# Performance work log

Hardware: AMD Instinct MI355X
Metric: run time of the kernel (lower is better)

The kernel has to match this reference:

```python
import jax, jax.numpy as jnp
import numpy as np

N, E, D, H, L, FF = 50000, 500000, 128, 8, 2, 512
HD = D // H  # head dim = 16


def setup_inputs() -> dict:
    key = jax.random.key(0)
    ks = jax.random.split(key, 16)
    inp = {
        "x": jax.random.normal(ks[0], (N, D), jnp.float32),
        "edge_index": jax.random.randint(ks[1], (2, E), 0, N, jnp.int32),
    }
    def w(k, shape, fan_in):
        return jax.random.normal(k, shape, jnp.float32) / np.float32(np.sqrt(fan_in))
    inp["Wq"] = w(ks[2], (L, D, D), D)
    inp["Wk"] = w(ks[3], (L, D, D), D)
    inp["Wv"] = w(ks[4], (L, D, D), D)
    inp["Wo"] = w(ks[5], (L, D, D), D)
    inp["Wpos"] = w(ks[6], (L, D, D), D)
    inp["Wdeg"] = w(ks[7], (L, 1, D), 1)
    inp["W1"] = w(ks[8], (L, D, FF), D)
    inp["W2"] = w(ks[9], (L, FF, D), FF)
    for name, shape in [("bq", (L, D)), ("bk", (L, D)), ("bv", (L, D)),
                        ("bo", (L, D)), ("bpos", (L, D)), ("bdeg", (L, D)),
                        ("ln1_b", (L, D)), ("ln2_b", (L, D)),
                        ("b1", (L, FF)), ("b2", (L, D))]:
        inp[name] = jnp.zeros(shape, jnp.float32)
    inp["ln1_g"] = jnp.ones((L, D), jnp.float32)
    inp["ln2_g"] = jnp.ones((L, D), jnp.float32)
    return inp


def _layernorm(x, g, b):
    mu = jnp.mean(x, axis=-1, keepdims=True)
    var = jnp.mean(jnp.square(x - mu), axis=-1, keepdims=True)
    return (x - mu) * jax.lax.rsqrt(var + 1e-5) * g + b


def _forward(edge_index, x, Wq, bq, Wk, bk, Wv, bv, Wo, bo, Wpos, bpos,
             Wdeg, bdeg, ln1_g, ln1_b, ln2_g, ln2_b, W1, b1, W2, b2):
    n = x.shape[0]
    loops = jnp.arange(n, dtype=edge_index.dtype)
    src = jnp.concatenate([edge_index[0], loops])  # [E+N]
    dst = jnp.concatenate([edge_index[1], loops])  # [E+N]
    scale = np.float32(np.sqrt(HD))
    for l in range(L):
        # pre-attention LayerNorm
        xn = _layernorm(x, ln1_g[l], ln1_b[l])
        # positional encoding: x + proj(x) + deg_proj(standardized degree)
        deg = jax.ops.segment_sum(jnp.ones_like(src, dtype=x.dtype), src, num_segments=n)
        deg = (deg - deg.mean()) / (jnp.std(deg, ddof=1) + 1e-6)
        pos = xn @ Wpos[l] + bpos[l] + deg[:, None] * Wdeg[l][0] + bdeg[l]
        xp = xn + pos
        # per-node QKV projections (linear => identical to per-edge projection)
        q = (xp @ Wq[l] + bq[l]).reshape(n, H, HD)
        k = (xp @ Wk[l] + bk[l]).reshape(n, H, HD)
        v = (xp @ Wv[l] + bv[l]).reshape(n, H, HD)
        # per-edge attention logits  [E+N, H]
        att = jnp.einsum('ehd,ehd->eh', q[dst], k[src]) / scale
        att = jnp.nan_to_num(jnp.clip(att, -50.0, 50.0), nan=0.0, posinf=50.0, neginf=-50.0)
        # segment softmax over destination nodes (every node has a self loop)
        m = jax.ops.segment_max(att, dst, num_segments=n)        # [N, H]
        ex = jnp.exp(att - m[dst])
        s = jax.ops.segment_sum(ex, dst, num_segments=n)
        alpha = ex / (s[dst] + 1e-16)                             # [E+N, H]
        # weighted aggregation + output projection
        msg = (v[src] * alpha[:, :, None]).reshape(-1, D)         # [E+N, D]
        aggr = jax.ops.segment_sum(msg, dst, num_segments=n)      # [N, D]
        x = x + (aggr @ Wo[l] + bo[l])
        # FFN sublayer
        h = jax.nn.gelu(_layernorm(x, ln2_g[l], ln2_b[l]) @ W1[l] + b1[l], approximate=False)
        x = x + (h @ W2[l] + b2[l])
    return x


def reference(x, edge_index, Wq, bq, Wk, bk, Wv, bv, Wo, bo, Wpos, bpos,
              Wdeg, bdeg, ln1_g, ln1_b, ln2_g, ln2_b, W1, b1, W2, b2):
    return _forward(edge_index, x, Wq, bq, Wk, bk, Wv, bv, Wo, bo, Wpos, bpos,
                    Wdeg, bdeg, ln1_g, ln1_b, ln2_g, ln2_b, W1, b1, W2, b2)
```

## Files before the change

### kernel.cpp

```cpp
#include <hip/hip_runtime.h>
#include <hip/hip_bf16.h>
#include <hip/hip_fp16.h>
#include <math.h>

#define DMODEL 128
#define NHEAD 8
#define HEADD 16
#define NLAYER 2
#define FFDIM 512
#define MPAD 50048
#define QKVW 384

using short8 = __attribute__((ext_vector_type(8))) short;
using half8  = __attribute__((ext_vector_type(8))) _Float16;
using f32x4  = __attribute__((ext_vector_type(4))) float;

static __device__ __forceinline__ unsigned short f2h(float f) {
    __half h = __float2half(f);
    unsigned short u; __builtin_memcpy(&u, &h, 2); return u;
}
static __device__ __forceinline__ float h2f(unsigned short u) {
    __half h; __builtin_memcpy(&h, &u, 2); return __half2float(h);
}
static __device__ __forceinline__ half8 s2h8(short8 s) {
    half8 h; __builtin_memcpy(&h, &s, 16); return h;
}
static __device__ __forceinline__ f32x4 MFMAH(short8 a, short8 b, f32x4 c) {
    return __builtin_amdgcn_mfma_f32_16x16x32_f16(s2h8(a), s2h8(b), c, 0, 0, 0);
}
static __device__ __forceinline__ float gelu_fast(float v) {
    float u = v * (0.7978845608f + 0.0356774081f * v * v);
    float t = 1.0f - 2.0f / (1.0f + __expf(2.0f * u));
    return 0.5f * v * (1.0f + t);
}

__global__ __launch_bounds__(256)
void ln_kernel(const float* __restrict__ x, const float* __restrict__ g,
               const float* __restrict__ b, unsigned short* __restrict__ out, int n)
{
    int wave = threadIdx.x >> 6;
    int lane = threadIdx.x & 63;
    int row  = blockIdx.x * 4 + wave;
    if (row >= n) return;
    float2 xv = *(const float2*)(x + (size_t)row * DMODEL + lane * 2);
    float s  = xv.x + xv.y;
    float ss = xv.x * xv.x + xv.y * xv.y;
    #pragma unroll
    for (int d = 1; d < 64; d <<= 1) {
        s  += __shfl_xor(s, d);
        ss += __shfl_xor(ss, d);
    }
    float mu   = s * (1.0f / 128.0f);
    float var  = ss * (1.0f / 128.0f) - mu * mu;
    float rstd = rsqrtf(var + 1e-5f);
    float2 gv = *(const float2*)(g + lane * 2);
    float2 bv = *(const float2*)(b + lane * 2);
    ushort2 o;
    o.x = f2h((xv.x - mu) * rstd * gv.x + bv.x);
    o.y = f2h((xv.y - mu) * rstd * gv.y + bv.y);
    *(ushort2*)(out + (size_t)row * DMODEL + lane * 2) = o;
}

__global__ void wconv(const float* __restrict__ W, unsigned short* __restrict__ Wt,
                      int K, int N, int total, int NR, int rowOff)
{
    int i = blockIdx.x * 256 + threadIdx.x;
    if (i >= total) return;
    int kn = K * N;
    int l = i / kn;
    int r = i - l * kn;
    int k = r / N;
    int nn = r - k * N;
    Wt[(size_t)l * NR * K + (size_t)(rowOff + nn) * K + k] = f2h(W[i]);
}

template<int MODE, int KCH, int TPB>
__global__ __launch_bounds__(256)
void gemm_bres(const unsigned short* __restrict__ A, int strideA,
               const unsigned short* __restrict__ Bt, int strideB,
               const float* __restrict__ bias, const float* __restrict__ bias2,
               const float* __restrict__ bias3,
               const unsigned short* __restrict__ Rb,
               const float* __restrict__ degs, const float* __restrict__ wdeg,
               const float* __restrict__ bdeg,
               float* __restrict__ outf, unsigned short* __restrict__ outb,
               int outStride, int n)
{
    __shared__ __align__(16) unsigned short As[64 * 130];
    __shared__ __align__(16) unsigned short Bs[128 * 130];

    const int tid  = threadIdx.x;
    const int wave = tid >> 6, lane = tid & 63;
    const int wr = wave >> 1, wc = wave & 1;
    const int quad = lane >> 4, l15 = lane & 15;
    const int bc = blockIdx.y * 128;

    f32x4 acc[2][4] = {};
    short8 bfr[4][4];
    short8 pr[4];

    {
        const int row0 = blockIdx.x * TPB * 64;
        #pragma unroll
        for (int c = 0; c < 4; ++c) {
            int g = tid + c * 256;
            int r = g >> 4, col8 = g & 15;
            pr[c] = *(const short8*)(A + (size_t)(row0 + r) * strideA + col8 * 8);
        }
    }

    for (int ky = 0; ky < KCH; ++ky) {
        const int kOff = ky * 128;
        #pragma unroll
        for (int c = 0; c < 8; ++c) {
            int g = tid + c * 256;
            int r = g >> 4, col8 = g & 15;
            *(short8*)&Bs[r * 130 + col8 * 8] =
                *(const short8*)(Bt + (size_t)(bc + r) * strideB + kOff + col8 * 8);
        }
        for (int t = 0; t < TPB; ++t) {
            #pragma unroll
            for (int c = 0; c < 4; ++c) {
                int g = tid + c * 256;
                int r = g >> 4, col8 = g & 15;
                *(short8*)&As[r * 130 + col8 * 8] = pr[c];
            }
            {
                int nt = t + 1, nky = ky;
                if (nt == TPB) { nt = 0; nky = ky + 1; }
                if (nky < KCH) {
                    const int nrow0 = (blockIdx.x * TPB + nt) * 64;
                    const int nkOff = nky * 128;
                    #pragma unroll
                    for (int c = 0; c < 4; ++c) {
                        int g = tid + c * 256;
                        int r = g >> 4, col8 = g & 15;
                        pr[c] = *(const short8*)(A + (size_t)(nrow0 + r) * strideA + nkOff + col8 * 8);
                    }
                }
            }
            __syncthreads();
            if (t == 0) {
                #pragma unroll
                for (int j = 0; j < 4; ++j)
                    #pragma unroll
                    for (int ks = 0; ks < 4; ++ks)
                        bfr[j][ks] = *(const short8*)&Bs[(wc * 64 + j * 16 + l15) * 130 + (ks * 4 + quad) * 8];
            }
            if (KCH == 1) {
                #pragma unroll
                for (int i = 0; i < 2; ++i)
                    #pragma unroll
                    for (int j = 0; j < 4; ++j)
                        acc[i][j] = f32x4{0.f, 0.f, 0.f, 0.f};
            }
            short8 af[2][4];
            #pragma unroll
            for (int i = 0; i < 2; ++i)
                #pragma unroll
                for (int ks = 0; ks < 4; ++ks)
                    af[i][ks] = *(const short8*)&As[(wr * 32 + i * 16 + l15) * 130 + (ks * 4 + quad) * 8];
            #pragma unroll
            for (int ks = 0; ks < 4; ++ks)
                #pragma unroll
                for (int i = 0; i < 2; ++i)
                    #pragma unroll
                    for (int j = 0; j < 4; ++j)
                        acc[i][j] = MFMAH(af[i][ks], bfr[j][ks], acc[i][j]);

            if (KCH == 1) {
                const int row0 = (blockIdx.x * TPB + t) * 64;
                #pragma unroll
                for (int i = 0; i < 2; ++i) {
                    #pragma unroll
                    for (int rr = 0; rr < 4; ++rr) {
                        size_t gr = (size_t)row0 + wr * 32 + i * 16 + quad * 4 + rr;
                        if (gr >= (size_t)n) continue;
                        #pragma unroll
                        for (int j = 0; j < 4; ++j) {
                            int col = wc * 64 + j * 16 + l15;
                            int gc  = bc + col;
                            float val = acc[i][j][rr];
                            if (MODE == 0) {
                                int sec = blockIdx.y;
                                const float* bp = (sec == 0) ? bias : (sec == 1 ? bias2 : bias3);
                                val += bp[col];
                                int idx = (sec == 0) ? col
                                        : (128 + ((col >> 1) << 2) + ((sec - 1) << 1) + (col & 1));
                                outb[gr * (size_t)QKVW + idx] = f2h(val);
                            } else if (MODE == 1) {
                                float* px = outf + gr * (size_t)outStride + gc;
                                *px = *px + val + bias[gc];
                            } else if (MODE == 2) {
                                val = gelu_fast(val + bias[gc]);
                                outb[gr * (size_t)outStride + gc] = f2h(val);
                            } else if (MODE == 3) {
                                val += bias[gc] + h2f(Rb[gr * (size_t)outStride + gc])
                                     + degs[gr] * wdeg[gc] + bdeg[gc];
                                outb[gr * (size_t)outStride + gc] = f2h(val);
                            }
                        }
                    }
                }
            }
            __syncthreads();
        }
    }

    if (KCH > 1) {
        const int row0 = blockIdx.x * TPB * 64;
        #pragma unroll
        for (int i = 0; i < 2; ++i) {
            #pragma unroll
            for (int rr = 0; rr < 4; ++rr) {
                size_t gr = (size_t)row0 + wr * 32 + i * 16 + quad * 4 + rr;
                if (gr >= (size_t)n) continue;
                #pragma unroll
                for (int j = 0; j < 4; ++j) {
                    int col = wc * 64 + j * 16 + l15;
                    int gc  = bc + col;
                    float val = acc[i][j][rr];
                    if (MODE == 1) {
                        float* px = outf + gr * (size_t)outStride + gc;
                        *px = *px + val + bias[gc];
                    }
                }
            }
        }
    }
}

__global__ void deg_init(float* __restrict__ deg, int n)
{
    int i = blockIdx.x * 256 + threadIdx.x;
    if (i < n) deg[i] = 1.0f;
}

__global__ void deg_count(const int* __restrict__ src, float* __restrict__ deg, int e)
{
    int i = blockIdx.x * 256 + threadIdx.x;
    if (i < e) atomicAdd(&deg[src[i]], 1.0f);
}

__global__ __launch_bounds__(256)
void deg_var(const float* __restrict__ deg, float* __restrict__ stats, float mean, int n)
{
    float acc = 0.f;
    for (int i = blockIdx.x * blockDim.x + threadIdx.x; i < n; i += gridDim.x * blockDim.x) {
        float d = deg[i] - mean;
        acc += d * d;
    }
    #pragma unroll
    for (int d = 1; d < 64; d <<= 1) acc += __shfl_xor(acc, d);
    __shared__ float wsum[4];
    int lane = threadIdx.x & 63, wv = threadIdx.x >> 6;
    if (lane == 0) wsum[wv] = acc;
    __syncthreads();
    if (threadIdx.x == 0) atomicAdd(stats, wsum[0] + wsum[1] + wsum[2] + wsum[3]);
}

__global__ void deg_norm(const float* __restrict__ deg, const float* __restrict__ stats,
                         float* __restrict__ degs, float mean, int n)
{
    int i = blockIdx.x * 256 + threadIdx.x;
    if (i >= n) return;
    float sd = sqrtf(stats[0] / (float)(n - 1));
    degs[i] = (deg[i] - mean) / (sd + 1e-6f);
}

__global__ void csr_count(const int* __restrict__ ei, int* __restrict__ counts, int e, int n)
{
    int i = blockIdx.x * 256 + threadIdx.x;
    if (i >= e + n) return;
    int d = (i < e) ? ei[e + i] : (i - e);
    atomicAdd(&counts[d], 1);
}

__global__ __launch_bounds__(256)
void scan_block(const int* __restrict__ in, int* __restrict__ out,
                int* __restrict__ sums, int n)
{
    __shared__ int buf[2][256];
    int t = threadIdx.x;
    int i = blockIdx.x * 256 + t;
    int v = (i < n) ? in[i] : 0;
    buf[0][t] = v;
    __syncthreads();
    int cur = 0;
    #pragma unroll
    for (int d = 1; d < 256; d <<= 1) {
        int val = buf[cur][t] + ((t >= d) ? buf[cur][t - d] : 0);
        buf[cur ^ 1][t] = val;
        cur ^= 1;
        __syncthreads();
    }
    if (i < n) out[i] = buf[cur][t] - v;
    if (t == 255 && sums) sums[blockIdx.x] = buf[cur][255];
}

__global__ void scan_add(int* __restrict__ offs, const int* __restrict__ carry, int n)
{
    int i = blockIdx.x * 256 + threadIdx.x;
    if (i < n) offs[i] += carry[blockIdx.x];
}

__global__ void csr_fill(const int* __restrict__ ei, const int* __restrict__ offs,
                         int* __restrict__ cursor, int* __restrict__ csr_src, int e, int n)
{
    int i = blockIdx.x * 256 + threadIdx.x;
    if (i >= e + n) return;
    int d, s;
    if (i < e) { s = ei[i]; d = ei[e + i]; }
    else       { s = d = i - e; }
    int pos = offs[d] + atomicAdd(&cursor[d], 1);
    csr_src[pos] = s;
}

__global__ __launch_bounds__(256)
void attn_kernel(const unsigned short* __restrict__ qkv,
                 const int* __restrict__ csr_src, const int* __restrict__ offs,
                 const int* __restrict__ counts,
                 unsigned short* __restrict__ aggr, int n)
{
    int wave = threadIdx.x >> 6;
    int lane = threadIdx.x & 63;
    int node = blockIdx.x * 4 + wave;
    if (node >= n) return;

    ushort2 qu = *(const ushort2*)(qkv + (size_t)node * QKVW + lane * 2);
    float qx = h2f(qu.x), qy = h2f(qu.y);
    int beg = offs[node], cnt = counts[node];

    float m = -1e30f, s = 0.f, ax = 0.f, ay = 0.f;
    ushort4 kvA = {0,0,0,0}, kvB = {0,0,0,0};
    if (cnt > 1) {
        int j0 = csr_src[beg], j1 = csr_src[beg + 1];
        kvA = *(const ushort4*)(qkv + (size_t)j0 * QKVW + DMODEL + lane * 4);
        kvB = *(const ushort4*)(qkv + (size_t)j1 * QKVW + DMODEL + lane * 4);
    } else {
        int j0 = csr_src[beg];
        kvA = *(const ushort4*)(qkv + (size_t)j0 * QKVW + DMODEL + lane * 4);
    }
    int t = 0;
    for (; t + 1 < cnt; t += 2) {
        ushort4 k0 = kvA, k1 = kvB;
        int rem = cnt - t - 2;
        if (rem >= 2) {
            int j0 = csr_src[beg + t + 2], j1 = csr_src[beg + t + 3];
            kvA = *(const ushort4*)(qkv + (size_t)j0 * QKVW + DMODEL + lane * 4);
            kvB = *(const ushort4*)(qkv + (size_t)j1 * QKVW + DMODEL + lane * 4);
        } else if (rem == 1) {
            int j0 = csr_src[beg + t + 2];
            kvA = *(const ushort4*)(qkv + (size_t)j0 * QKVW + DMODEL + lane * 4);
        }
        float p0 = qx * h2f(k0.x) + qy * h2f(k0.y);
        float p1 = qx * h2f(k1.x) + qy * h2f(k1.y);
        p0 += __shfl_xor(p0, 1); p1 += __shfl_xor(p1, 1);
        p0 += __shfl_xor(p0, 2); p1 += __shfl_xor(p1, 2);
        p0 += __shfl_xor(p0, 4); p1 += __shfl_xor(p1, 4);
        p0 *= 0.25f; p1 *= 0.25f;
        p0 = (p0 != p0) ? 0.f : fminf(fmaxf(p0, -50.f), 50.f);
        p1 = (p1 != p1) ? 0.f : fminf(fmaxf(p1, -50.f), 50.f);
        float nm = fmaxf(m, fmaxf(p0, p1));
        float sc = __expf(m - nm);
        float e0 = __expf(p0 - nm), e1 = __expf(p1 - nm);
        s  = s  * sc + e0 + e1;
        ax = ax * sc + e0 * h2f(k0.z) + e1 * h2f(k1.z);
        ay = ay * sc + e0 * h2f(k0.w) + e1 * h2f(k1.w);
        m = nm;
    }
    if (t < cnt) {
        float p0 = qx * h2f(kvA.x) + qy * h2f(kvA.y);
        p0 += __shfl_xor(p0, 1); p0 += __shfl_xor(p0, 2); p0 += __shfl_xor(p0, 4);
        p0 *= 0.25f;
        p0 = (p0 != p0) ? 0.f : fminf(fmaxf(p0, -50.f), 50.f);
        float nm = fmaxf(m, p0);
        float sc = __expf(m - nm), e0 = __expf(p0 - nm);
        s = s * sc + e0;
        ax = ax * sc + e0 * h2f(kvA.z);
        ay = ay * sc + e0 * h2f(kvA.w);
        m = nm;
    }
    float r = 1.0f / (s + 1e-16f);
    ushort2 o;
    o.x = f2h(ax * r);
    o.y = f2h(ay * r);
    *(ushort2*)(aggr + (size_t)node * DMODEL + lane * 2) = o;
}

extern "C" void kernel_launch(void* const* d_in, const int* in_sizes, int n_in,
                              void* d_out, int out_size, void* d_ws, size_t ws_size,
                              hipStream_t stream)
{
    const float* x_in  = (const float*)d_in[0];
    const int*   ei    = (const int*)d_in[1];
    const float* Wq    = (const float*)d_in[2];
    const float* Wk    = (const float*)d_in[3];
    const float* Wv    = (const float*)d_in[4];
    const float* Wo    = (const float*)d_in[5];
    const float* Wpos  = (const float*)d_in[6];
    const float* Wdeg  = (const float*)d_in[7];
    const float* W1    = (const float*)d_in[8];
    const float* W2    = (const float*)d_in[9];
    const float* bq    = (const float*)d_in[10];
    const float* bk    = (const float*)d_in[11];
    const float* bv    = (const float*)d_in[12];
    const float* bo    = (const float*)d_in[13];
    const float* bpos  = (const float*)d_in[14];
    const float* bdeg  = (const float*)d_in[15];
    const float* ln1_b = (const float*)d_in[16];
    const float* ln2_b = (const float*)d_in[17];
    const float* b1    = (const float*)d_in[18];
    const float* b2    = (const float*)d_in[19];
    const float* ln1_g = (const float*)d_in[20];
    const float* ln2_g = (const float*)d_in[21];

    const int n   = in_sizes[0] / DMODEL;
    const int e   = in_sizes[1] / 2;
    const int tot = e + n;

    float* x = (float*)d_out;

    char* p = (char*)d_ws;
    auto alloc = [&](size_t bytes) -> void* {
        void* r = (void*)p;
        p += (bytes + 255) & ~(size_t)255;
        return r;
    };
    float* deg     = (float*)alloc((size_t)n * 4);
    float* degs    = (float*)alloc((size_t)n * 4);
    float* stats   = (float*)alloc(256);
    int*   counts  = (int*)alloc((size_t)n * 4);
    int*   offs    = (int*)alloc((size_t)n * 4);
    int*   cursor  = (int*)alloc((size_t)n * 4);
    int*   bsums   = (int*)alloc(1024);
    int*   carry   = (int*)alloc(1024);
    int*   csr_src = (int*)alloc((size_t)tot * 4);
    unsigned short* xnb  = (unsigned short*)alloc((size_t)MPAD * DMODEL * 2);
    unsigned short* xp   = (unsigned short*)alloc((size_t)MPAD * DMODEL * 2);
    unsigned short* aggr = (unsigned short*)alloc((size_t)MPAD * DMODEL * 2);
    unsigned short* qkv  = (unsigned short*)alloc((size_t)MPAD * QKVW * 2);
    unsigned short* hb   = (unsigned short*)alloc((size_t)MPAD * FFDIM * 2);
    unsigned short* wqkvt = (unsigned short*)alloc((size_t)NLAYER * QKVW * DMODEL * 2);
    unsigned short* wot  = (unsigned short*)alloc((size_t)NLAYER * DMODEL * DMODEL * 2);
    unsigned short* wpt  = (unsigned short*)alloc((size_t)NLAYER * DMODEL * DMODEL * 2);
    unsigned short* w1t  = (unsigned short*)alloc((size_t)NLAYER * DMODEL * FFDIM * 2);
    unsigned short* w2t  = (unsigned short*)alloc((size_t)NLAYER * FFDIM * DMODEL * 2);

    const int nb_n = (n + 255) / 256;
    const int nb_e = (e + 255) / 256;
    const int nb_t = (tot + 255) / 256;
    const int nscan = nb_n;

    hipMemcpyAsync(x, x_in, (size_t)n * DMODEL * 4, hipMemcpyDeviceToDevice, stream);
    hipMemsetAsync(stats, 0, 256, stream);
    hipMemsetAsync(counts, 0, (size_t)n * 4, stream);
    hipMemsetAsync(cursor, 0, (size_t)n * 4, stream);

    {
        int tDD = NLAYER * DMODEL * DMODEL;
        int tW1 = NLAYER * DMODEL * FFDIM;
        wconv<<<(tDD + 255) / 256, 256, 0, stream>>>(Wq,   wqkvt, DMODEL, DMODEL, tDD, QKVW, 0);
        wconv<<<(tDD + 255) / 256, 256, 0, stream>>>(Wk,   wqkvt, DMODEL, DMODEL, tDD, QKVW, 128);
        wconv<<<(tDD + 255) / 256, 256, 0, stream>>>(Wv,   wqkvt, DMODEL, DMODEL, tDD, QKVW, 256);
        wconv<<<(tDD + 255) / 256, 256, 0, stream>>>(Wo,   wot, DMODEL, DMODEL, tDD, DMODEL, 0);
        wconv<<<(tDD + 255) / 256, 256, 0, stream>>>(Wpos, wpt, DMODEL, DMODEL, tDD, DMODEL, 0);
        wconv<<<(tW1 + 255) / 256, 256, 0, stream>>>(W1,   w1t, DMODEL, FFDIM,  tW1, FFDIM, 0);
        wconv<<<(tW1 + 255) / 256, 256, 0, stream>>>(W2,   w2t, FFDIM,  DMODEL, tW1, DMODEL, 0);
    }

    const float mean = (float)((double)tot / (double)n);
    deg_init<<<nb_n, 256, 0, stream>>>(deg, n);
    deg_count<<<nb_e, 256, 0, stream>>>(ei, deg, e);
    deg_var<<<196, 256, 0, stream>>>(deg, stats, mean, n);
    deg_norm<<<nb_n, 256, 0, stream>>>(deg, stats, degs, mean, n);

    csr_count<<<nb_t, 256, 0, stream>>>(ei, counts, e, n);
    scan_block<<<nscan, 256, 0, stream>>>(counts, offs, bsums, n);
    scan_block<<<1, 256, 0, stream>>>(bsums, carry, nullptr, nscan);
    scan_add<<<nscan, 256, 0, stream>>>(offs, carry, n);
    csr_fill<<<nb_t, 256, 0, stream>>>(ei, offs, cursor, csr_src, e, n);

    const int nTiles  = MPAD / 64;
    const int gx2     = nTiles / 2;
    const int ln_grid = (n + 3) / 4;

    for (int l = 0; l < NLAYER; ++l) {
        const size_t DD = (size_t)DMODEL * DMODEL;
        const float* wdeg = Wdeg + (size_t)l * DMODEL;
        const unsigned short* wqkv = wqkvt + (size_t)l * QKVW * DMODEL;
        const unsigned short* wo   = wot + l * DD;
        const unsigned short* wpos = wpt + l * DD;
        const unsigned short* w1   = w1t + (size_t)l * DMODEL * FFDIM;
        const unsigned short* w2   = w2t + (size_t)l * FFDIM * DMODEL;

        ln_kernel<<<ln_grid, 256, 0, stream>>>(x, ln1_g + l * DMODEL, ln1_b + l * DMODEL, xnb, n);
        gemm_bres<3, 1, 2><<<dim3(gx2, 1), 256, 0, stream>>>(
            xnb, DMODEL, wpos, DMODEL,
            bpos + l * DMODEL, nullptr, nullptr,
            xnb, degs, wdeg, bdeg + l * DMODEL,
            nullptr, xp, DMODEL, n);
        gemm_bres<0, 1, 2><<<dim3(gx2, 3), 256, 0, stream>>>(
            xp, DMODEL, wqkv, DMODEL,
            bq + l * DMODEL, bk + l * DMODEL, bv + l * DMODEL,
            nullptr, nullptr, nullptr, nullptr,
            nullptr, qkv, QKVW, n);
        attn_kernel<<<ln_grid, 256, 0, stream>>>(qkv, csr_src, offs, counts, aggr, n);
        gemm_bres<1, 1, 2><<<dim3(gx2, 1), 256, 0, stream>>>(
            aggr, DMODEL, wo, DMODEL,
            bo + l * DMODEL, nullptr, nullptr,
            nullptr, nullptr, nullptr, nullptr,
            x, nullptr, DMODEL, n);
        ln_kernel<<<ln_grid, 256, 0, stream>>>(x, ln2_g + l * DMODEL, ln2_b + l * DMODEL, xnb, n);
        gemm_bres<2, 1, 2><<<dim3(gx2, 4), 256, 0, stream>>>(
            xnb, DMODEL, w1, DMODEL,
            b1 + l * FFDIM, nullptr, nullptr,
            nullptr, nullptr, nullptr, nullptr,
            nullptr, hb, FFDIM, n);
        gemm_bres<1, 4, 1><<<dim3(nTiles, 1), 256, 0, stream>>>(
            hb, FFDIM, w2, FFDIM,
            b2 + l * DMODEL, nullptr, nullptr,
            nullptr, nullptr, nullptr, nullptr,
            x, nullptr, DMODEL, n);
    }
}
```

Baseline: 619.2 us.

## Fuse LayerNorm into residual GEMM epilogues and merge setup kernels

Adds a GEMM epilogue mode that applies the residual add and then LayerNorm over the full 128-wide row, using a shared-memory reduction across waves. The separate LayerNorm kernels after the Wo and W2 GEMMs go away, which removes an extra full read of x per LayerNorm. The setup work is also consolidated: the weight conversions become one kernel, the memsets and degree init become one kernel, and degree normalization moves into the positional GEMM epilogue. The attention loop is rewritten to process four edges per iteration with prefetching of the next group and no NaN check. The cost is an extra block sync and more register pressure in the GEMM epilogue.

```diff
diff --git a/kernel.cpp b/kernel.cpp
--- a/kernel.cpp
+++ b/kernel.cpp
@@ -61,17 +61,173 @@
     *(ushort2*)(out + (size_t)row * DMODEL + lane * 2) = o;
 }
 
-__global__ void wconv(const float* __restrict__ W, unsigned short* __restrict__ Wt,
-                      int K, int N, int total, int NR, int rowOff)
-{
+__global__ void wconv_all(const float* __restrict__ Wq, const float* __restrict__ Wk,
+                          const float* __restrict__ Wv, const float* __restrict__ Wo,
+                          const float* __restrict__ Wpos, const float* __restrict__ W1,
+                          const float* __restrict__ W2,
+                          unsigned short* __restrict__ wqkvt, unsigned short* __restrict__ wot,
+                          unsigned short* __restrict__ wpt, unsigned short* __restrict__ w1t,
+                          unsigned short* __restrict__ w2t)
+{
+    const int DD = NLAYER * DMODEL * DMODEL;
+    const int DF = NLAYER * DMODEL * FFDIM;
     int i = blockIdx.x * 256 + threadIdx.x;
-    if (i >= total) return;
-    int kn = K * N;
-    int l = i / kn;
-    int r = i - l * kn;
-    int k = r / N;
-    int nn = r - k * N;
-    Wt[(size_t)l * NR * K + (size_t)(rowOff + nn) * K + k] = f2h(W[i]);
+    if (i < 3 * DD) {
+        int w = i / DD, r = i - w * DD;
+        const float* src = (w == 0) ? Wq : (w == 1 ? Wk : Wv);
+        int l = r >> 14, rr = r & 16383;
+        int k = rr >> 7, nn = rr & 127;
+        wqkvt[(size_t)l * QKVW * DMODEL + (size_t)(w * 128 + nn) * DMODEL + k] = f2h(src[r]);
+    } else if (i < 5 * DD) {
+        int w = (i - 3 * DD) / DD, r = (i - 3 * DD) - w * DD;
+        const float* src = (w == 0) ? Wo : Wpos;
+        unsigned short* dst = (w == 0) ? wot : wpt;
+        int l = r >> 14, rr = r & 16383;
+        int k = rr >> 7, nn = rr & 127;
+        dst[(size_t)l * DMODEL * DMODEL + (size_t)nn * DMODEL + k] = f2h(src[r]);
+    } else if (i < 5 * DD + DF) {
+        int r = i - 5 * DD;
+        int l = r >> 16, rr = r & 65535;
+        int k = rr >> 9, nn = rr & 511;
+        w1t[(size_t)l * FFDIM * DMODEL + (size_t)nn * DMODEL + k] = f2h(W1[r]);
+    } else if (i < 5 * DD + 2 * DF) {
+        int r = i - 5 * DD - DF;
+        int l = r >> 16, rr = r & 65535;
+        int k = rr >> 7, nn = rr & 127;
+        w2t[(size_t)l * DMODEL * FFDIM + (size_t)nn * FFDIM + k] = f2h(W2[r]);
+    }
+}
+
+__global__ void init_all(float* __restrict__ deg, int* __restrict__ counts,
+                         int* __restrict__ cursor, float* __restrict__ stats, int n)
+{
+    int i = blockIdx.x * 256 + threadIdx.x;
+    if (i < n) { deg[i] = 1.0f; counts[i] = 0; cursor[i] = 0; }
+    if (i == 0) stats[0] = 0.f;
+}
+
+__global__ void deg_count(const int* __restrict__ src, float* __restrict__ deg, int e)
+{
+    int i = blockIdx.x * 256 + threadIdx.x;
+    if (i < e) atomicAdd(&deg[src[i]], 1.0f);
+}
+
+__global__ __launch_bounds__(256)
+void deg_var(const float* __restrict__ deg, float* __restrict__ stats, float mean, int n)
+{
+    float acc = 0.f;
+    for (int i = blockIdx.x * blockDim.x + threadIdx.x; i < n; i += gridDim.x * blockDim.x) {
+        float d = deg[i] - mean;
+        acc += d * d;
+    }
+    #pragma unroll
+    for (int d = 1; d < 64; d <<= 1) acc += __shfl_xor(acc, d);
+    __shared__ float wsum[4];
+    int lane = threadIdx.x & 63, wv = threadIdx.x >> 6;
+    if (lane == 0) wsum[wv] = acc;
+    __syncthreads();
+    if (threadIdx.x == 0) atomicAdd(stats, wsum[0] + wsum[1] + wsum[2] + wsum[3]);
+}
+
+__global__ void csr_count(const int* __restrict__ ei, int* __restrict__ counts, int e, int n)
+{
+    int i = blockIdx.x * 256 + threadIdx.x;
+    if (i >= e + n) return;
+    int d = (i < e) ? ei[e + i] : (i - e);
+    atomicAdd(&counts[d], 1);
+}
+
+__global__ __launch_bounds__(256)
+void scan_block(const int* __restrict__ in, int* __restrict__ out,
+                int* __restrict__ sums, int n)
+{
+    __shared__ int buf[2][256];
+    int t = threadIdx.x;
+    int i = blockIdx.x * 256 + t;
+    int v = (i < n) ? in[i] : 0;
+    buf[0][t] = v;
+    __syncthreads();
+    int cur = 0;
+    #pragma unroll
+    for (int d = 1; d < 256; d <<= 1) {
+        int val = buf[cur][t] + ((t >= d) ? buf[cur][t - d] : 0);
+        buf[cur ^ 1][t] = val;
+        cur ^= 1;
+        __syncthreads();
+    }
+    if (i < n) out[i] = buf[cur][t] - v;
+    if (t == 255 && sums) sums[blockIdx.x] = buf[cur][255];
+}
+
+__global__ void scan_add(int* __restrict__ offs, const int* __restrict__ carry, int n)
+{
+    int i = blockIdx.x * 256 + threadIdx.x;
+    if (i < n) offs[i] += carry[blockIdx.x];
+}
+
+__global__ void csr_fill(const int* __restrict__ ei, const int* __restrict__ offs,
+                         int* __restrict__ cursor, int* __restrict__ csr_src, int e, int n)
+{
+    int i = blockIdx.x * 256 + threadIdx.x;
+    if (i >= e + n) return;
+    int d, s;
+    if (i < e) { s = ei[i]; d = ei[e + i]; }
+    else       { s = d = i - e; }
+    int pos = offs[d] + atomicAdd(&cursor[d], 1);
+    csr_src[pos] = s;
+}
+
+static __device__ __forceinline__ void ep_resln(
+    f32x4 (&acc)[2][4], float* sm, int row0,
+    int wr, int wc, int quad, int l15,
+    const float* __restrict__ bias, const float* __restrict__ g,
+    const float* __restrict__ bb,
+    float* __restrict__ x, unsigned short* __restrict__ lnout, int n)
+{
+    #pragma unroll
+    for (int i = 0; i < 2; ++i) {
+        #pragma unroll
+        for (int rr = 0; rr < 4; ++rr) {
+            int rl = wr * 32 + i * 16 + quad * 4 + rr;
+            size_t gr = (size_t)row0 + rl;
+            float ps = 0.f, pq = 0.f;
+            #pragma unroll
+            for (int j = 0; j < 4; ++j) {
+                int gc = wc * 64 + j * 16 + l15;
+                float xv = (gr < (size_t)n) ? x[gr * DMODEL + gc] : 0.f;
+                float v = acc[i][j][rr] + bias[gc] + xv;
+                acc[i][j][rr] = v;
+                ps += v; pq += v * v;
+            }
+            ps += __shfl_xor(ps, 1); pq += __shfl_xor(pq, 1);
+            ps += __shfl_xor(ps, 2); pq += __shfl_xor(pq, 2);
+            ps += __shfl_xor(ps, 4); pq += __shfl_xor(pq, 4);
+            ps += __shfl_xor(ps, 8); pq += __shfl_xor(pq, 8);
+            if (l15 == 0) { sm[(rl * 2 + wc) * 2 + 0] = ps; sm[(rl * 2 + wc) * 2 + 1] = pq; }
+        }
+    }
+    __syncthreads();
+    #pragma unroll
+    for (int i = 0; i < 2; ++i) {
+        #pragma unroll
+        for (int rr = 0; rr < 4; ++rr) {
+            int rl = wr * 32 + i * 16 + quad * 4 + rr;
+            size_t gr = (size_t)row0 + rl;
+            if (gr >= (size_t)n) continue;
+            float su = sm[(rl * 2 + 0) * 2 + 0] + sm[(rl * 2 + 1) * 2 + 0];
+            float sq = sm[(rl * 2 + 0) * 2 + 1] + sm[(rl * 2 + 1) * 2 + 1];
+            float mu   = su * (1.f / 128.f);
+            float var  = sq * (1.f / 128.f) - mu * mu;
+            float rstd = rsqrtf(var + 1e-5f);
+            #pragma unroll
+            for (int j = 0; j < 4; ++j) {
+                int gc = wc * 64 + j * 16 + l15;
+                float v = acc[i][j][rr];
+                x[gr * DMODEL + gc] = v;
+                lnout[gr * DMODEL + gc] = f2h((v - mu) * rstd * g[gc] + bb[gc]);
+            }
+        }
+    }
 }
 
 template<int MODE, int KCH, int TPB>
@@ -81,13 +237,15 @@
                const float* __restrict__ bias, const float* __restrict__ bias2,
                const float* __restrict__ bias3,
                const unsigned short* __restrict__ Rb,
-               const float* __restrict__ degs, const float* __restrict__ wdeg,
-               const float* __restrict__ bdeg,
+               const float* __restrict__ deg, const float* __restrict__ stats, float mean,
+               const float* __restrict__ wdeg, const float* __restrict__ bdeg,
+               const float* __restrict__ lng, const float* __restrict__ lnb,
                float* __restrict__ outf, unsigned short* __restrict__ outb,
                int outStride, int n)
 {
     __shared__ __align__(16) unsigned short As[64 * 130];
     __shared__ __align__(16) unsigned short Bs[128 * 130];
+    __shared__ float sm[64 * 2 * 2];
 
     const int tid  = threadIdx.x;
     const int wave = tid >> 6, lane = tid & 63;
@@ -170,34 +328,41 @@
 
             if (KCH == 1) {
                 const int row0 = (blockIdx.x * TPB + t) * 64;
-                #pragma unroll
-                for (int i = 0; i < 2; ++i) {
+                if (MODE == 5) {
+                    ep_resln(acc, sm, row0, wr, wc, quad, l15, bias, lng, lnb, outf, outb, n);
+                } else {
+                    float sdv = 0.f;
+                    if (MODE == 3) sdv = sqrtf(stats[0] / (float)(n - 1)) + 1e-6f;
                     #pragma unroll
-                    for (int rr = 0; rr < 4; ++rr) {
-                        size_t gr = (size_t)row0 + wr * 32 + i * 16 + quad * 4 + rr;
-                        if (gr >= (size_t)n) continue;
+                    for (int i = 0; i < 2; ++i) {
                         #pragma unroll
-                        for (int j = 0; j < 4; ++j) {
-                            int col = wc * 64 + j * 16 + l15;
-                            int gc  = bc + col;
-                            float val = acc[i][j][rr];
-                            if (MODE == 0) {
-                                int sec = blockIdx.y;
-                                const float* bp = (sec == 0) ? bias : (sec == 1 ? bias2 : bias3);
-                                val += bp[col];
-                                int idx = (sec == 0) ? col
-                                        : (128 + ((col >> 1) << 2) + ((sec - 1) << 1) + (col & 1));
-                                outb[gr * (size_t)QKVW + idx] = f2h(val);
-                            } else if (MODE == 1) {
-                                float* px = outf + gr * (size_t)outStride + gc;
-                                *px = *px + val + bias[gc];
-                            } else if (MODE == 2) {
-                                val = gelu_fast(val + bias[gc]);
-                                outb[gr * (size_t)outStride + gc] = f2h(val);
-                            } else if (MODE == 3) {
-                                val += bias[gc] + h2f(Rb[gr * (size_t)outStride + gc])
-                                     + degs[gr] * wdeg[gc] + bdeg[gc];
-                                outb[gr * (size_t)outStride + gc] = f2h(val);
+                        for (int rr = 0; rr < 4; ++rr) {
+                            size_t gr = (size_t)row0 + wr * 32 + i * 16 + quad * 4 + rr;
+                            if (gr >= (size_t)n) continue;
+                            #pragma unroll
+                            for (int j = 0; j < 4; ++j) {
+                                int col = wc * 64 + j * 16 + l15;
+                                int gc  = bc + col;
+                                float val = acc[i][j][rr];
+                                if (MODE == 0) {
+                                    int sec = blockIdx.y;
+                                    const float* bp = (sec == 0) ? bias : (sec == 1 ? bias2 : bias3);
+                                    val += bp[col];
+                                    int idx = (sec == 0) ? col
+                                            : (128 + ((col >> 1) << 2) + ((sec - 1) << 1) + (col & 1));
+                                    outb[gr * (size_t)QKVW + idx] = f2h(val);
+                                } else if (MODE == 1) {
+                                    float* px = outf + gr * (size_t)outStride + gc;
+                                    *px = *px + val + bias[gc];
+                                } else if (MODE == 2) {
+                                    val = gelu_fast(val + bias[gc]);
+                                    outb[gr * (size_t)outStride + gc] = f2h(val);
+                                } else if (MODE == 3) {
+                                    float dg = (deg[gr] - mean) / sdv;
+                                    val += bias[gc] + h2f(Rb[gr * (size_t)outStride + gc])
+                                         + dg * wdeg[gc] + bdeg[gc];
+                                    outb[gr * (size_t)outStride + gc] = f2h(val);
+                                }
                             }
                         }
                     }
@@ -209,111 +374,28 @@
 
     if (KCH > 1) {
         const int row0 = blockIdx.x * TPB * 64;
-        #pragma unroll
-        for (int i = 0; i < 2; ++i) {
+        if (MODE == 5) {
+            ep_resln(acc, sm, row0, wr, wc, quad, l15, bias, lng, lnb, outf, outb, n);
+        } else {
             #pragma unroll
-            for (int rr = 0; rr < 4; ++rr) {
-                size_t gr = (size_t)row0 + wr * 32 + i * 16 + quad * 4 + rr;
-                if (gr >= (size_t)n) continue;
+            for (int i = 0; i < 2; ++i) {
                 #pragma unroll
-                for (int j = 0; j < 4; ++j) {
-                    int col = wc * 64 + j * 16 + l15;
-                    int gc  = bc + col;
-                    float val = acc[i][j][rr];
-                    if (MODE == 1) {
-                        float* px = outf + gr * (size_t)outStride + gc;
-                        *px = *px + val + bias[gc];
+                for (int rr = 0; rr < 4; ++rr) {
+                    size_t gr = (size_t)row0 + wr * 32 + i * 16 + quad * 4 + rr;
+                    if (gr >= (size_t)n) continue;
+                    #pragma unroll
+                    for (int j = 0; j < 4; ++j) {
+                        int col = wc * 64 + j * 16 + l15;
+                        int gc  = bc + col;
+                        if (MODE == 1) {
+                            float* px = outf + gr * (size_t)outStride + gc;
+                            *px = *px + acc[i][j][rr] + bias[gc];
+                        }
                     }
                 }
             }
         }
     }
-}
-
-__global__ void deg_init(float* __restrict__ deg, int n)
-{
-    int i = blockIdx.x * 256 + threadIdx.x;
-    if (i < n) deg[i] = 1.0f;
-}
-
-__global__ void deg_count(const int* __restrict__ src, float* __restrict__ deg, int e)
-{
-    int i = blockIdx.x * 256 + threadIdx.x;
-    if (i < e) atomicAdd(&deg[src[i]], 1.0f);
-}
-
-__global__ __launch_bounds__(256)
-void deg_var(const float* __restrict__ deg, float* __restrict__ stats, float mean, int n)
-{
-    float acc = 0.f;
-    for (int i = blockIdx.x * blockDim.x + threadIdx.x; i < n; i += gridDim.x * blockDim.x) {
-        float d = deg[i] - mean;
-        acc += d * d;
-    }
-    #pragma unroll
-    for (int d = 1; d < 64; d <<= 1) acc += __shfl_xor(acc, d);
-    __shared__ float wsum[4];
-    int lane = threadIdx.x & 63, wv = threadIdx.x >> 6;
-    if (lane == 0) wsum[wv] = acc;
-    __syncthreads();
-    if (threadIdx.x == 0) atomicAdd(stats, wsum[0] + wsum[1] + wsum[2] + wsum[3]);
-}
-
-__global__ void deg_norm(const float* __restrict__ deg, const float* __restrict__ stats,
-                         float* __restrict__ degs, float mean, int n)
-{
-    int i = blockIdx.x * 256 + threadIdx.x;
-    if (i >= n) return;
-    float sd = sqrtf(stats[0] / (float)(n - 1));
-    degs[i] = (deg[i] - mean) / (sd + 1e-6f);
-}
-
-__global__ void csr_count(const int* __restrict__ ei, int* __restrict__ counts, int e, int n)
-{
-    int i = blockIdx.x * 256 + threadIdx.x;
-    if (i >= e + n) return;
-    int d = (i < e) ? ei[e + i] : (i - e);
-    atomicAdd(&counts[d], 1);
-}
-
-__global__ __launch_bounds__(256)
-void scan_block(const int* __restrict__ in, int* __restrict__ out,
-                int* __restrict__ sums, int n)
-{
-    __shared__ int buf[2][256];
-    int t = threadIdx.x;
-    int i = blockIdx.x * 256 + t;
-    int v = (i < n) ? in[i] : 0;
-    buf[0][t] = v;
-    __syncthreads();
-    int cur = 0;
-    #pragma unroll
-    for (int d = 1; d < 256; d <<= 1) {
-        int val = buf[cur][t] + ((t >= d) ? buf[cur][t - d] : 0);
-        buf[cur ^ 1][t] = val;
-        cur ^= 1;
-        __syncthreads();
-    }
-    if (i < n) out[i] = buf[cur][t] - v;
-    if (t == 255 && sums) sums[blockIdx.x] = buf[cur][255];
-}
-
-__global__ void scan_add(int* __restrict__ offs, const int* __restrict__ carry, int n)
-{
-    int i = blockIdx.x * 256 + threadIdx.x;
-    if (i < n) offs[i] += carry[blockIdx.x];
-}
-
-__global__ void csr_fill(const int* __restrict__ ei, const int* __restrict__ offs,
-                         int* __restrict__ cursor, int* __restrict__ csr_src, int e, int n)
-{
-    int i = blockIdx.x * 256 + threadIdx.x;
-    if (i >= e + n) return;
-    int d, s;
-    if (i < e) { s = ei[i]; d = ei[e + i]; }
-    else       { s = d = i - e; }
-    int pos = offs[d] + atomicAdd(&cursor[d], 1);
-    csr_src[pos] = s;
 }
 
 __global__ __launch_bounds__(256)
@@ -331,60 +413,64 @@
     float qx = h2f(qu.x), qy = h2f(qu.y);
     int beg = offs[node], cnt = counts[node];
 
+    const unsigned short* base = qkv + DMODEL + lane * 4;
+    auto LKV = [&](int t) -> ushort4 {
+        return *(const ushort4*)(base + (size_t)csr_src[beg + t] * QKVW);
+    };
+
     float m = -1e30f, s = 0.f, ax = 0.f, ay = 0.f;
-    ushort4 kvA = {0,0,0,0}, kvB = {0,0,0,0};
-    if (cnt > 1) {
-        int j0 = csr_src[beg], j1 = csr_src[beg + 1];
-        kvA = *(const ushort4*)(qkv + (size_t)j0 * QKVW + DMODEL + lane * 4);
-        kvB = *(const ushort4*)(qkv + (size_t)j1 * QKVW + DMODEL + lane * 4);
-    } else {
-        int j0 = csr_src[beg];
-        kvA = *(const ushort4*)(qkv + (size_t)j0 * QKVW + DMODEL + lane * 4);
-    }
+    ushort4 k0 = {0,0,0,0}, k1 = {0,0,0,0}, k2 = {0,0,0,0}, k3 = {0,0,0,0};
+    k0 = LKV(0);
+    if (cnt > 1) k1 = LKV(1);
+    if (cnt > 2) k2 = LKV(2);
+    if (cnt > 3) k3 = LKV(3);
+
     int t = 0;
-    for (; t + 1 < cnt; t += 2) {
-        ushort4 k0 = kvA, k1 = kvB;
-        int rem = cnt - t - 2;
-        if (rem >= 2) {
-            int j0 = csr_src[beg + t + 2], j1 = csr_src[beg + t + 3];
-            kvA = *(const ushort4*)(qkv + (size_t)j0 * QKVW + DMODEL + lane * 4);
-            kvB = *(const ushort4*)(qkv + (size_t)j1 * QKVW + DMODEL + lane * 4);
-        } else if (rem == 1) {
-            int j0 = csr_src[beg + t + 2];
-            kvA = *(const ushort4*)(qkv + (size_t)j0 * QKVW + DMODEL + lane * 4);
-        }
-        float p0 = qx * h2f(k0.x) + qy * h2f(k0.y);
-        float p1 = qx * h2f(k1.x) + qy * h2f(k1.y);
-        p0 += __shfl_xor(p0, 1); p1 += __shfl_xor(p1, 1);
-        p0 += __shfl_xor(p0, 2); p1 += __shfl_xor(p1, 2);
-        p0 += __shfl_xor(p0, 4); p1 += __shfl_xor(p1, 4);
-        p0 *= 0.25f; p1 *= 0.25f;
-        p0 = (p0 != p0) ? 0.f : fminf(fmaxf(p0, -50.f), 50.f);
-        p1 = (p1 != p1) ? 0.f : fminf(fmaxf(p1, -50.f), 50.f);
-        float nm = fmaxf(m, fmaxf(p0, p1));
+    for (; t + 4 <= cnt; t += 4) {
+        ushort4 c0 = k0, c1 = k1, c2 = k2, c3 = k3;
+        int rem = cnt - t - 4;
+        if (rem > 0) k0 = LKV(t + 4);
+        if (rem > 1) k1 = LKV(t + 5);
+        if (rem > 2) k2 = LKV(t + 6);
+        if (rem > 3) k3 = LKV(t + 7);
+        float p0 = qx * h2f(c0.x) + qy * h2f(c0.y);
+        float p1 = qx * h2f(c1.x) + qy * h2f(c1.y);
+        float p2 = qx * h2f(c2.x) + qy * h2f(c2.y);
+        float p3 = qx * h2f(c3.x) + qy * h2f(c3.y);
+        p0 += __shfl_xor(p0, 1); p1 += __shfl_xor(p1, 1); p2 += __shfl_xor(p2, 1); p3 += __shfl_xor(p3, 1);
+        p0 += __shfl_xor(p0, 2); p1 += __shfl_xor(p1, 2); p2 += __shfl_xor(p2, 2); p3 += __shfl_xor(p3, 2);
+        p0 += __shfl_xor(p0, 4); p1 += __shfl_xor(p1, 4); p2 += __shfl_xor(p2, 4); p3 += __shfl_xor(p3, 4);
+        p0 = fminf(fmaxf(p0 * 0.25f, -50.f), 50.f);
+        p1 = fminf(fmaxf(p1 * 0.25f, -50.f), 50.f);
+        p2 = fminf(fmaxf(p2 * 0.25f, -50.f), 50.f);
+        p3 = fminf(fmaxf(p3 * 0.25f, -50.f), 50.f);
+        float nm = fmaxf(m, fmaxf(fmaxf(p0, p1), fmaxf(p2, p3)));
         float sc = __expf(m - nm);
         float e0 = __expf(p0 - nm), e1 = __expf(p1 - nm);
-        s  = s  * sc + e0 + e1;
-        ax = ax * sc + e0 * h2f(k0.z) + e1 * h2f(k1.z);
-        ay = ay * sc + e0 * h2f(k0.w) + e1 * h2f(k1.w);
+        float e2 = __expf(p2 - nm), e3 = __expf(p3 - nm);
+        s  = s  * sc + ((e0 + e1) + (e2 + e3));
+        ax = ax * sc + e0 * h2f(c0.z) + e1 * h2f(c1.z) + e2 * h2f(c2.z) + e3 * h2f(c3.z);
+        ay = ay * sc + e0 * h2f(c0.w) + e1 * h2f(c1.w) + e2 * h2f(c2.w) + e3 * h2f(c3.w);
         m = nm;
     }
-    if (t < cnt) {
-        float p0 = qx * h2f(kvA.x) + qy * h2f(kvA.y);
-        p0 += __shfl_xor(p0, 1); p0 += __shfl_xor(p0, 2); p0 += __shfl_xor(p0, 4);
-        p0 *= 0.25f;
-        p0 = (p0 != p0) ? 0.f : fminf(fmaxf(p0, -50.f), 50.f);
-        float nm = fmaxf(m, p0);
-        float sc = __expf(m - nm), e0 = __expf(p0 - nm);
-        s = s * sc + e0;
-        ax = ax * sc + e0 * h2f(kvA.z);
-        ay = ay * sc + e0 * h2f(kvA.w);
-        m = nm;
-    }
-    float r = 1.0f / (s + 1e-16f);
+    int r = cnt - t;
+    #define ONE_EDGE(kc) do { \
+        float p = qx * h2f(kc.x) + qy * h2f(kc.y); \
+        p += __shfl_xor(p, 1); p += __shfl_xor(p, 2); p += __shfl_xor(p, 4); \
+        p = fminf(fmaxf(p * 0.25f, -50.f), 50.f); \
+        float nm = fmaxf(m, p); \
+        float sc = __expf(m - nm), e = __expf(p - nm); \
+        s = s * sc + e; ax = ax * sc + e * h2f(kc.z); ay = ay * sc + e * h2f(kc.w); \
+        m = nm; } while (0)
+    if (r > 0) ONE_EDGE(k0);
+    if (r > 1) ONE_EDGE(k1);
+    if (r > 2) ONE_EDGE(k2);
+    #undef ONE_EDGE
+
+    float rcp = 1.0f / (s + 1e-16f);
     ushort2 o;
-    o.x = f2h(ax * r);
-    o.y = f2h(ay * r);
+    o.x = f2h(ax * rcp);
+    o.y = f2h(ay * rcp);
     *(ushort2*)(aggr + (size_t)node * DMODEL + lane * 2) = o;
 }
 
@@ -428,7 +514,6 @@
         return r;
     };
     float* deg     = (float*)alloc((size_t)n * 4);
-    float* degs    = (float*)alloc((size_t)n * 4);
     float* stats   = (float*)alloc(256);
     int*   counts  = (int*)alloc((size_t)n * 4);
     int*   offs    = (int*)alloc((size_t)n * 4);
@@ -453,27 +538,17 @@
     const int nscan = nb_n;
 
     hipMemcpyAsync(x, x_in, (size_t)n * DMODEL * 4, hipMemcpyDeviceToDevice, stream);
-    hipMemsetAsync(stats, 0, 256, stream);
-    hipMemsetAsync(counts, 0, (size_t)n * 4, stream);
-    hipMemsetAsync(cursor, 0, (size_t)n * 4, stream);
 
     {
-        int tDD = NLAYER * DMODEL * DMODEL;
-        int tW1 = NLAYER * DMODEL * FFDIM;
-        wconv<<<(tDD + 255) / 256, 256, 0, stream>>>(Wq,   wqkvt, DMODEL, DMODEL, tDD, QKVW, 0);
-        wconv<<<(tDD + 255) / 256, 256, 0, stream>>>(Wk,   wqkvt, DMODEL, DMODEL, tDD, QKVW, 128);
-        wconv<<<(tDD + 255) / 256, 256, 0, stream>>>(Wv,   wqkvt, DMODEL, DMODEL, tDD, QKVW, 256);
-        wconv<<<(tDD + 255) / 256, 256, 0, stream>>>(Wo,   wot, DMODEL, DMODEL, tDD, DMODEL, 0);
-        wconv<<<(tDD + 255) / 256, 256, 0, stream>>>(Wpos, wpt, DMODEL, DMODEL, tDD, DMODEL, 0);
-        wconv<<<(tW1 + 255) / 256, 256, 0, stream>>>(W1,   w1t, DMODEL, FFDIM,  tW1, FFDIM, 0);
-        wconv<<<(tW1 + 255) / 256, 256, 0, stream>>>(W2,   w2t, FFDIM,  DMODEL, tW1, DMODEL, 0);
-    }
+        const int totalW = 5 * NLAYER * DMODEL * DMODEL + 2 * NLAYER * DMODEL * FFDIM;
+        wconv_all<<<(totalW + 255) / 256, 256, 0, stream>>>(Wq, Wk, Wv, Wo, Wpos, W1, W2,
+                                                            wqkvt, wot, wpt, w1t, w2t);
+    }
+    init_all<<<nb_n, 256, 0, stream>>>(deg, counts, cursor, stats, n);
 
     const float mean = (float)((double)tot / (double)n);
-    deg_init<<<nb_n, 256, 0, stream>>>(deg, n);
     deg_count<<<nb_e, 256, 0, stream>>>(ei, deg, e);
     deg_var<<<196, 256, 0, stream>>>(deg, stats, mean, n);
-    deg_norm<<<nb_n, 256, 0, stream>>>(deg, stats, degs, mean, n);
 
     csr_count<<<nb_t, 256, 0, stream>>>(ei, counts, e, n);
     scan_block<<<nscan, 256, 0, stream>>>(counts, offs, bsums, n);
@@ -484,6 +559,8 @@
     const int nTiles  = MPAD / 64;
     const int gx2     = nTiles / 2;
     const int ln_grid = (n + 3) / 4;
+
+    ln_kernel<<<ln_grid, 256, 0, stream>>>(x, ln1_g, ln1_b, xnb, n);
 
     for (int l = 0; l < NLAYER; ++l) {
         const size_t DD = (size_t)DMODEL * DMODEL;
@@ -494,33 +571,45 @@
         const unsigned short* w1   = w1t + (size_t)l * DMODEL * FFDIM;
         const unsigned short* w2   = w2t + (size_t)l * FFDIM * DMODEL;
 
-        ln_kernel<<<ln_grid, 256, 0, stream>>>(x, ln1_g + l * DMODEL, ln1_b + l * DMODEL, xnb, n);
         gemm_bres<3, 1, 2><<<dim3(gx2, 1), 256, 0, stream>>>(
             xnb, DMODEL, wpos, DMODEL,
             bpos + l * DMODEL, nullptr, nullptr,
-            xnb, degs, wdeg, bdeg + l * DMODEL,
+            xnb, deg, stats, mean, wdeg, bdeg + l * DMODEL,
+            nullptr, nullptr,
             nullptr, xp, DMODEL, n);
         gemm_bres<0, 1, 2><<<dim3(gx2, 3), 256, 0, stream>>>(
             xp, DMODEL, wqkv, DMODEL,
             bq + l * DMODEL, bk + l * DMODEL, bv + l * DMODEL,
-            nullptr, nullptr, nullptr, nullptr,
+            nullptr, nullptr, nullptr, 0.f, nullptr, nullptr,
+            nullptr, nullptr,
             nullptr, qkv, QKVW, n);
         attn_kernel<<<ln_grid, 256, 0, stream>>>(qkv, csr_src, offs, counts, aggr, n);
-        gemm_bres<1, 1, 2><<<dim3(gx2, 1), 256, 0, stream>>>(
+        gemm_bres<5, 1, 2><<<dim3(gx2, 1), 256, 0, stream>>>(
             aggr, DMODEL, wo, DMODEL,
             bo + l * DMODEL, nullptr, nullptr,
-            nullptr, nullptr, nullptr, nullptr,
-            x, nullptr, DMODEL, n);
-        ln_kernel<<<ln_grid, 256, 0, stream>>>(x, ln2_g + l * DMODEL, ln2_b + l * DMODEL, xnb, n);
+            nullptr, nullptr, nullptr, 0.f, nullptr, nullptr,
+            ln2_g + l * DMODEL, ln2_b + l * DMODEL,
+            x, xnb, DMODEL, n);
         gemm_bres<2, 1, 2><<<dim3(gx2, 4), 256, 0, stream>>>(
             xnb, DMODEL, w1, DMODEL,
             b1 + l * FFDIM, nullptr, nullptr,
-            nullptr, nullptr, nullptr, nullptr,
+            nullptr, nullptr, nullptr, 0.f, nullptr, nullptr,
+            nullptr, nullptr,
             nullptr, hb, FFDIM, n);
-        gemm_bres<1, 4, 1><<<dim3(nTiles, 1), 256, 0, stream>>>(
-            hb, FFDIM, w2, FFDIM,
-            b2 + l * DMODEL, nullptr, nullptr,
-            nullptr, nullptr, nullptr, nullptr,
-            x, nullptr, DMODEL, n);
-    }
-}
+        if (l + 1 < NLAYER) {
+            gemm_bres<5, 4, 1><<<dim3(nTiles, 1), 256, 0, stream>>>(
+                hb, FFDIM, w2, FFDIM,
+                b2 + l * DMODEL, nullptr, nullptr,
+                nullptr, nullptr, nullptr, 0.f, nullptr, nullptr,
+                ln1_g + (l + 1) * DMODEL, ln1_b + (l + 1) * DMODEL,
+                x, xnb, DMODEL, n);
+        } else {
+            gemm_bres<1, 4, 1><<<dim3(nTiles, 1), 256, 0, stream>>>(
+                hb, FFDIM, w2, FFDIM,
+                b2 + l * DMODEL, nullptr, nullptr,
+                nullptr, nullptr, nullptr, 0.f, nullptr, nullptr,
+                nullptr, nullptr,
+                x, nullptr, DMODEL, n);
+        }
+    }
+}
```

Result: slower. 636.6 us (+2.8%).
